# Performance work log

Hardware: AMD Instinct MI355X
Metric: run time of the kernel (lower is better)

The kernel has to match this reference:

```python
import jax, jax.numpy as jnp
import numpy as np

ANCHORS = jnp.array([[0.57273, 0.677385], [1.87446, 2.06253], [3.33843, 5.47434],
                     [7.88282, 3.52778], [9.77052, 9.16828]], dtype=jnp.float32)
IOU_THR = 0.6
SCALE_NOOBJ = 1.0
SCALE_OBJ = 5.0
DS = 32.0          # downsample_rate
EPS = 1e-7


def _iou_wh(w1, h1, w2, h2):
    # GetCenterAlignIouBetween: boxes aligned at centers -> IoU depends on w,h only
    inter = jnp.minimum(w1, w2) * jnp.minimum(h1, h2)
    return inter / (w1 * h1 + w2 * h2 - inter + EPS)


def setup_inputs() -> dict:
    B, W, H, A, C, M = 128, 19, 19, 5, 81, 24
    N = W * H
    key = jax.random.key(0)
    ks = jax.random.split(key, 8)
    ii, jj = jnp.meshgrid(jnp.arange(W), jnp.arange(H), indexing='ij')
    fm_cord = jnp.stack([jj, ii], -1).reshape(N, 2).astype(jnp.float32)  # (x=j, y=i)
    conf = jax.random.uniform(ks[0], (B, W, H, A, 1)) * 0.98 + 0.01      # valid BCE probs
    pred_xy = fm_cord.reshape(1, W, H, 1, 2) + jax.random.uniform(ks[1], (B, W, H, A, 2))
    pred_wh = jax.random.uniform(ks[2], (B, W, H, A, 2)) * 8.0 + 0.2     # fm units, >0
    cls_score = jax.random.normal(ks[3], (B, W, H, A, C))
    # distinct grid cells per image so sequential scatter == vectorized scatter
    cells = jax.vmap(lambda k: jax.random.choice(k, N, (M,), replace=False))(
        jax.random.split(ks[4], B))
    ci = cells // H
    cj = cells % H
    frac = jax.random.uniform(ks[5], (B, M, 2))
    x = (cj.astype(jnp.float32) + frac[..., 0]) * DS   # pixel coords
    y = (ci.astype(jnp.float32) + frac[..., 1]) * DS
    wh = jax.random.uniform(ks[6], (B, M, 2), minval=12.0, maxval=280.0)
    true_object = jnp.stack([x, y, wh[..., 0], wh[..., 1]], -1)          # [B,M,4] pixels
    labels = jax.random.randint(ks[7], (B, M), 0, C - 1)
    true_label = jax.nn.one_hot(labels, C, dtype=jnp.float32)            # [B,M,C]
    return dict(epoch=0, conf=conf, pred_xy=pred_xy, pred_wh=pred_wh,
                cls_score=cls_score, true_label=true_label,
                true_object=true_object, fm_cord=fm_cord)


def _yolo_loss(conf, pred_xy, pred_wh, cls_score, true_label, true_object, fm_cord):
    B, W, H, A, C = cls_score.shape
    N = W * H
    NA = N * A
    S = float(W)  # config.output_size

    # ---- target assignment (vectorized version of the python loops) ----
    obj = true_object / DS                               # fm units, [B,M,4]
    gx, gy, gw, gh = obj[..., 0], obj[..., 1], obj[..., 2], obj[..., 3]
    i = gy.astype(jnp.int32)                             # row index  (int() truncation)
    j = gx.astype(jnp.int32)                             # col index
    cell = i * H + j                                     # flat cell, [B,M]

    a_iou = _iou_wh(ANCHORS[None, None, :, 0], ANCHORS[None, None, :, 1],
                    gw[..., None], gh[..., None])        # [B,M,A]
    best = jnp.argmax(a_iou, axis=-1)                    # [B,M]
    is_best = best[..., None] == jnp.arange(A)[None, None, :]
    over = a_iou > IOU_THR

    bb = jnp.arange(B)[:, None]
    pwh = pred_wh.reshape(B, N, A, 2)[bb, cell]          # [B,M,A,2] gather at gt cells
    pwh_b = jnp.take_along_axis(pwh, best[..., None, None], axis=2)[:, :, 0]  # [B,M,2]
    iou_pg = _iou_wh(pwh_b[..., 0], pwh_b[..., 1], gw, gh)                    # [B,M]

    mask_val = jnp.where(is_best, 1.0, jnp.where(over, -1.0, 0.0))            # [B,M,A]
    sw = 2.0 - (gw / S) * (gh / S)                                            # [B,M]
    sw_val = jnp.where(is_best, sw[..., None], jnp.where(over, -1.0, 0.0))
    pgi_val = jnp.where(~is_best & over, 0.0, iou_pg[..., None])              # [B,M,A]
    bg = jax.nn.one_hot(C - 1, C, dtype=cls_score.dtype)
    ts_val = jnp.where((is_best | over)[..., None], true_label[:, :, None, :], bg)
    bbox_val = jnp.where(is_best[..., None], obj[:, :, None, :], 0.0)         # [B,M,A,4]

    obj_mask = jnp.zeros((B, N, A)).at[bb, cell].set(mask_val)
    scale_w = jnp.zeros((B, N, A)).at[bb, cell].set(sw_val)
    pgi = jnp.zeros((B, N, A)).at[bb, cell].set(pgi_val)
    true_score = jnp.zeros((B, N, A, C)).at[..., -1].set(1.0).at[bb, cell].set(ts_val)
    true_bbox = jnp.zeros((B, N, A, 4)).at[bb, cell].set(bbox_val)

    # ---- masked losses over flattened [B, W*H*A, ...] ----
    conf_f = conf.reshape(B, NA)
    om = obj_mask.reshape(B, NA)
    swf = scale_w.reshape(B, NA)
    pgif = pgi.reshape(B, NA)
    pxy = pred_xy.reshape(B, NA, 2)
    pwh_f = pred_wh.reshape(B, NA, 2)
    tb = true_bbox.reshape(B, NA, 4)
    ts = true_score.reshape(B, NA, C)
    cs = cls_score.reshape(B, NA, C)
    cord = jnp.repeat(fm_cord[:, None, :], A, axis=1).reshape(NA, 2)

    cp = jnp.clip(conf_f, EPS, 1.0 - EPS)
    noobj_loss = SCALE_NOOBJ * jnp.sum((om == 0) * (-jnp.log(1.0 - cp))) / B
    obj_loss = SCALE_OBJ * jnp.sum(
        (om == 1) * (-(pgif * jnp.log(cp) + (1.0 - pgif) * jnp.log(1.0 - cp)))) / B

    gt = (swf > 0).astype(conf_f.dtype)                  # [B,NA]
    w3 = (SCALE_OBJ * gt * swf)[..., None]
    xy_loss = jnp.sum(w3 * ((pxy - cord[None]) - (tb[..., :2] - cord[None])) ** 2) / B
    wh_loss = jnp.sum(w3 * (pwh_f - tb[..., 2:]) ** 2) / B

    # CE with soft targets, per position: [B,NA]
    ce = -jnp.sum(ts * jax.nn.log_softmax(cs, axis=-1), axis=-1)
    # original broadcasts mask [B,1,NA] * ce [B,NA] -> [B,B,NA] then .sum();
    # equivalent factored form: sum_n (sum_b1 mask) * (sum_b2 ce)
    score_loss = SCALE_OBJ * jnp.sum(gt.sum(0) * ce.sum(0)) / B

    total = noobj_loss + obj_loss + xy_loss + wh_loss + score_loss
    return total, noobj_loss, obj_loss, score_loss, xy_loss, wh_loss


def reference(epoch, conf, pred_xy, pred_wh, cls_score, true_label, true_object, fm_cord):
    return _yolo_loss(conf, pred_xy, pred_wh, cls_score,
                      true_label, true_object, fm_cord)
```

## Files before the change

kernel.cpp:

```cpp
#include <hip/hip_runtime.h>

#define Bsz 128
#define Cd 81
#define Md 24
#define Nd 361
#define NAd 1805
#define RPW 16
#define NT 113
#define NBLK_CLS (NT*16)
#define NOBJ (Bsz*Md)
#define NBLK_LAB (NOBJ/RPW)
#define EPSF 1e-7f
#define IOU_THRF 0.6f

#define OFF_CORR  0
#define OFF_GT    1824
#define OFF_ACC   3648
#define MEMSET_FLOATS 3652
#define OFF_PART  4096
#define OFF_NOOBJ 33024
#define OFF_LAB   35072

#define EXP4(v) { v.x=__expf(v.x); v.y=__expf(v.y); v.z=__expf(v.z); v.w=__expf(v.w); }

__global__ __launch_bounds__(64) void yolo_sweep(
        const float* __restrict__ conf,
        const float* __restrict__ cls_score,
        const float* __restrict__ true_label,
        float* __restrict__ ws) {
    __shared__ float ex[1300];
    const int lane = threadIdx.x;
    const int r = lane >> 2, h = lane & 3;
    const int bid = blockIdx.x;
    float4* l4 = (float4*)ex;

    if (bid < NBLK_CLS) {
        const int t = bid >> 4, g = bid & 15;
        const int na0 = (t == NT - 1) ? (NAd - RPW) : t * RPW;
        const int vmin = t * RPW;
        const bool validr = (na0 + r) >= vmin;
        const bool validc = (lane < RPW) && ((na0 + lane) >= vmin);

        float accCE = 0.0f, nb = 0.0f;

        size_t s = ((size_t)(g * 8) * NAd + na0) * Cd;
        size_t a0 = s & ~(size_t)3;
        int mcur = (int)(s & 3);
        const float4* gp = (const float4*)cls_score + (a0 >> 2);
        float4 u0 = gp[0 * 64 + lane];
        float4 u1 = gp[1 * 64 + lane];
        float4 u2 = gp[2 * 64 + lane];
        float4 u3 = gp[3 * 64 + lane];
        float4 u4 = gp[4 * 64 + lane];
        float4 u5 = gp[261 + lane];
        float cf = validc ? conf[(size_t)(g * 8) * NAd + na0 + lane] : 0.5f;

        for (int it = 0; it < 8; ++it) {
            EXP4(u0); EXP4(u1); EXP4(u2); EXP4(u3); EXP4(u4); EXP4(u5);
            l4[0 * 64 + lane] = u0;
            l4[1 * 64 + lane] = u1;
            l4[2 * 64 + lane] = u2;
            l4[3 * 64 + lane] = u3;
            l4[4 * 64 + lane] = u4;
            l4[261 + lane] = u5;
            __builtin_amdgcn_wave_barrier();

            float4 n0 = {}, n1 = {}, n2 = {}, n3 = {}, n4 = {}, n5 = {};
            float cfn = 0.0f; int mnext = 0;
            if (it < 7) {
                int b = g * 8 + it + 1;
                s = ((size_t)b * NAd + na0) * Cd;
                a0 = s & ~(size_t)3;
                mnext = (int)(s & 3);
                gp = (const float4*)cls_score + (a0 >> 2);
                n0 = gp[0 * 64 + lane];
                n1 = gp[1 * 64 + lane];
                n2 = gp[2 * 64 + lane];
                n3 = gp[3 * 64 + lane];
                n4 = gp[4 * 64 + lane];
                n5 = gp[261 + lane];
                cfn = validc ? conf[(size_t)b * NAd + na0 + lane] : 0.5f;
            }

            const float* p = ex + mcur + r * Cd;
            float sacc = 0.0f;
            #pragma unroll
            for (int j = 0; j < 21; j++) {
                int c0 = h * 21 + j;
                int cc = c0 < 81 ? c0 : 80;
                float w = (c0 < 81) ? 1.0f : 0.0f;
                sacc += p[cc] * w;
            }
            sacc += __shfl_xor(sacc, 1, 64);
            sacc += __shfl_xor(sacc, 2, 64);
            if (h == 0 && validr)
                accCE += __logf(sacc) - __logf(p[80]);
            if (validc) {
                float cp = fminf(fmaxf(cf, EPSF), 1.0f - EPSF);
                nb += -__logf(1.0f - cp);
            }

            u0 = n0; u1 = n1; u2 = n2; u3 = n3; u4 = n4; u5 = n5;
            cf = cfn; mcur = mnext;
        }

        if (h == 0 && validr)
            ws[OFF_PART + (size_t)(na0 + r) * 16 + g] = accCE;

        #pragma unroll
        for (int off = 32; off > 0; off >>= 1) nb += __shfl_xor(nb, off, 64);
        if (lane == 0) ws[OFF_NOOBJ + bid] = nb;
    } else {
        const int lb = bid - NBLK_CLS;
        const float4* gp = (const float4*)(true_label + (size_t)lb * (RPW * Cd));
        float4 u0 = gp[0 * 64 + lane];
        float4 u1 = gp[1 * 64 + lane];
        float4 u2 = gp[2 * 64 + lane];
        float4 u3 = gp[3 * 64 + lane];
        float4 u4 = gp[4 * 64 + lane];
        float4 u5 = gp[260 + lane];
        l4[0 * 64 + lane] = u0;
        l4[1 * 64 + lane] = u1;
        l4[2 * 64 + lane] = u2;
        l4[3 * 64 + lane] = u3;
        l4[4 * 64 + lane] = u4;
        l4[260 + lane] = u5;
        __builtin_amdgcn_wave_barrier();
        const float* p = ex + r * Cd;
        float sacc = 0.0f;
        #pragma unroll
        for (int j = 0; j < 21; j++) {
            int c0 = h * 21 + j;
            int cc = c0 < 81 ? c0 : 80;
            float w = (c0 < 81) ? (float)c0 : 0.0f;
            sacc += p[cc] * w;
        }
        sacc += __shfl_xor(sacc, 1, 64);
        sacc += __shfl_xor(sacc, 2, 64);
        if (h == 0) ws[OFF_LAB + lb * RPW + r] = sacc;
    }
}

__global__ __launch_bounds__(64) void yolo_assign(
        const float* __restrict__ conf,
        const float* __restrict__ pred_xy,
        const float* __restrict__ pred_wh,
        const float* __restrict__ cls_score,
        const float* __restrict__ true_object,
        float* __restrict__ ws) {
    const float AW[5] = {0.57273f, 1.87446f, 3.33843f, 7.88282f, 9.77052f};
    const float AH[5] = {0.677385f, 2.06253f, 5.47434f, 3.52778f, 9.16828f};
    const int idx = blockIdx.x * 64 + threadIdx.x;
    float* corr = ws + OFF_CORR;
    float* gt   = ws + OFF_GT;

    int lab = (int)(ws[OFF_LAB + idx] + 0.5f);
    int b = idx / Md;
    const float4 to = ((const float4*)true_object)[idx];
    const float inv_ds = 1.0f / 32.0f;
    float gx = to.x * inv_ds, gy = to.y * inv_ds;
    float gw = to.z * inv_ds, gh = to.w * inv_ds;
    int ci = (int)gy, cj = (int)gx;
    int cell = ci * 19 + cj;
    float garea = gw * gh;

    float best_iou = -1.0f; int best = 0; bool over[5];
    #pragma unroll
    for (int a = 0; a < 5; a++) {
        float inter = fminf(AW[a], gw) * fminf(AH[a], gh);
        float iou = inter / (AW[a] * AH[a] + garea - inter + EPSF);
        over[a] = iou > IOU_THRF;
        if (iou > best_iou) { best_iou = iou; best = a; }
    }

    int base_bn = (b * Nd + cell) * 5;
    float pwb = pred_wh[(size_t)(base_bn + best) * 2 + 0];
    float phb = pred_wh[(size_t)(base_bn + best) * 2 + 1];
    float inter = fminf(pwb, gw) * fminf(phb, gh);
    float iou_pg = inter / (pwb * phb + garea - inter + EPSF);
    float sw = 2.0f - (gw * (1.0f / 19.0f)) * (gh * (1.0f / 19.0f));

    float a0 = 0.f, a1 = 0.f, a2 = 0.f, a3 = 0.f;
    #pragma unroll
    for (int a = 0; a < 5; a++) {
        bool isb = (a == best);
        if (!(isb || over[a])) continue;
        int pos = base_bn + a;
        int na  = cell * 5 + a;
        float cp = fminf(fmaxf(conf[pos], EPSF), 1.0f - EPSF);
        a0 += __logf(1.0f - cp);
        const float* cs = cls_score + (size_t)pos * Cd;
        atomicAdd(&corr[na], cs[Cd - 1] - cs[lab]);
        if (isb) {
            atomicAdd(&gt[na], 1.0f);
            a1 += -(iou_pg * __logf(cp) + (1.0f - iou_pg) * __logf(1.0f - cp));
            float px = pred_xy[(size_t)pos * 2 + 0], py = pred_xy[(size_t)pos * 2 + 1];
            a2 += sw * ((px - gx) * (px - gx) + (py - gy) * (py - gy));
            float pwa = pred_wh[(size_t)pos * 2 + 0], pha = pred_wh[(size_t)pos * 2 + 1];
            a3 += sw * ((pwa - gw) * (pwa - gw) + (pha - gh) * (pha - gh));
        }
    }

    #pragma unroll
    for (int off = 32; off > 0; off >>= 1) {
        a0 += __shfl_xor(a0, off, 64);
        a1 += __shfl_xor(a1, off, 64);
        a2 += __shfl_xor(a2, off, 64);
        a3 += __shfl_xor(a3, off, 64);
    }
    if (threadIdx.x == 0) {
        atomicAdd(&ws[OFF_ACC + 0], a0);
        atomicAdd(&ws[OFF_ACC + 1], a1);
        atomicAdd(&ws[OFF_ACC + 2], a2);
        atomicAdd(&ws[OFF_ACC + 3], a3);
    }
}

__global__ __launch_bounds__(1024) void yolo_reduce(
        const float* __restrict__ ws, float* __restrict__ out) {
    __shared__ float red[2][16];
    const int tid = threadIdx.x;
    float nsum = 0.0f;
    for (int i = tid; i < NBLK_CLS; i += 1024) nsum += ws[OFF_NOOBJ + i];
    float ssum = 0.0f;
    const float4* part4 = (const float4*)(ws + OFF_PART);
    for (int na = tid; na < NAd; na += 1024) {
        float4 p0 = part4[na * 4 + 0];
        float4 p1 = part4[na * 4 + 1];
        float4 p2 = part4[na * 4 + 2];
        float4 p3 = part4[na * 4 + 3];
        float ce = p0.x + p0.y + p0.z + p0.w + p1.x + p1.y + p1.z + p1.w
                 + p2.x + p2.y + p2.z + p2.w + p3.x + p3.y + p3.z + p3.w
                 + ws[OFF_CORR + na];
        ssum += ws[OFF_GT + na] * ce;
    }

    float v[2] = {nsum, ssum};
    #pragma unroll
    for (int k = 0; k < 2; k++) {
        float x = v[k];
        #pragma unroll
        for (int off = 32; off > 0; off >>= 1) x += __shfl_xor(x, off, 64);
        if ((tid & 63) == 0) red[k][tid >> 6] = x;
    }
    __syncthreads();
    if (tid == 0) {
        float t0 = 0.f, t1 = 0.f;
        #pragma unroll
        for (int w = 0; w < 16; w++) { t0 += red[0][w]; t1 += red[1][w]; }
        const float invB = 1.0f / (float)Bsz;
        float noobj = 1.0f * (t0 + ws[OFF_ACC + 0]) * invB;
        float obj   = 5.0f * ws[OFF_ACC + 1] * invB;
        float xy    = 5.0f * ws[OFF_ACC + 2] * invB;
        float wh    = 5.0f * ws[OFF_ACC + 3] * invB;
        float score = 5.0f * t1 * invB;
        out[0] = noobj + obj + xy + wh + score;
        out[1] = noobj;
        out[2] = obj;
        out[3] = score;
        out[4] = xy;
        out[5] = wh;
    }
}

extern "C" void kernel_launch(void* const* d_in, const int* in_sizes, int n_in,
                              void* d_out, int out_size, void* d_ws, size_t ws_size,
                              hipStream_t stream) {
    const float* conf    = (const float*)d_in[1];
    const float* pred_xy = (const float*)d_in[2];
    const float* pred_wh = (const float*)d_in[3];
    const float* cls     = (const float*)d_in[4];
    const float* tlabel  = (const float*)d_in[5];
    const float* tobject = (const float*)d_in[6];
    float* ws  = (float*)d_ws;
    float* out = (float*)d_out;

    hipMemsetAsync(ws, 0, MEMSET_FLOATS * sizeof(float), stream);

    yolo_sweep<<<NBLK_CLS + NBLK_LAB, 64, 0, stream>>>(conf, cls, tlabel, ws);

    yolo_assign<<<NOBJ / 64, 64, 0, stream>>>(conf, pred_xy, pred_wh, cls, tobject, ws);

    yolo_reduce<<<1, 1024, 0, stream>>>(ws, out);
}
```

Measured before the change: 131.7 us.

## Fuse target assignment into sweep kernel and halve per-block batch group

Merges the assign kernel into the class-score sweep kernel as leading blocks, computing each object's label index directly from its one-hot row instead of through a separate label-decoding pass and workspace buffer. This removes one kernel launch and the dependency between label decode and assignment. The sweep now covers 4 images per block instead of 8, doubling the block count to 32 groups per tile, with the partial-sum layout and final reduction widened to match. Each assign thread now reads a full 81-float label row serially with uncoalesced strided access. Smaller groups give more parallelism but less prefetch pipelining per block.

```diff
diff --git a/kernel.cpp b/kernel.cpp
--- a/kernel.cpp
+++ b/kernel.cpp
@@ -7,9 +7,11 @@
 #define NAd 1805
 #define RPW 16
 #define NT 113
-#define NBLK_CLS (NT*16)
+#define GPB 4
+#define NGRP 32
+#define NBLK_CLS (NT*NGRP)
 #define NOBJ (Bsz*Md)
-#define NBLK_LAB (NOBJ/RPW)
+#define NBLK_ASSIGN (NOBJ/64)
 #define EPSF 1e-7f
 #define IOU_THRF 0.6f
 
@@ -18,24 +20,27 @@
 #define OFF_ACC   3648
 #define MEMSET_FLOATS 3652
 #define OFF_PART  4096
-#define OFF_NOOBJ 33024
-#define OFF_LAB   35072
+#define OFF_NOOBJ 61952
 
 #define EXP4(v) { v.x=__expf(v.x); v.y=__expf(v.y); v.z=__expf(v.z); v.w=__expf(v.w); }
 
-__global__ __launch_bounds__(64) void yolo_sweep(
+__global__ __launch_bounds__(64) void yolo_main(
         const float* __restrict__ conf,
+        const float* __restrict__ pred_xy,
+        const float* __restrict__ pred_wh,
         const float* __restrict__ cls_score,
         const float* __restrict__ true_label,
+        const float* __restrict__ true_object,
         float* __restrict__ ws) {
     __shared__ float ex[1300];
     const int lane = threadIdx.x;
-    const int r = lane >> 2, h = lane & 3;
     const int bid = blockIdx.x;
-    float4* l4 = (float4*)ex;
-
-    if (bid < NBLK_CLS) {
-        const int t = bid >> 4, g = bid & 15;
+
+    if (bid >= NBLK_ASSIGN) {
+        const int cb = bid - NBLK_ASSIGN;
+        const int t = cb >> 5, g = cb & 31;
+        const int r = lane >> 2, h = lane & 3;
+        float4* l4 = (float4*)ex;
         const int na0 = (t == NT - 1) ? (NAd - RPW) : t * RPW;
         const int vmin = t * RPW;
         const bool validr = (na0 + r) >= vmin;
@@ -43,7 +48,7 @@
 
         float accCE = 0.0f, nb = 0.0f;
 
-        size_t s = ((size_t)(g * 8) * NAd + na0) * Cd;
+        size_t s = ((size_t)(g * GPB) * NAd + na0) * Cd;
         size_t a0 = s & ~(size_t)3;
         int mcur = (int)(s & 3);
         const float4* gp = (const float4*)cls_score + (a0 >> 2);
@@ -53,9 +58,9 @@
         float4 u3 = gp[3 * 64 + lane];
         float4 u4 = gp[4 * 64 + lane];
         float4 u5 = gp[261 + lane];
-        float cf = validc ? conf[(size_t)(g * 8) * NAd + na0 + lane] : 0.5f;
-
-        for (int it = 0; it < 8; ++it) {
+        float cf = validc ? conf[(size_t)(g * GPB) * NAd + na0 + lane] : 0.5f;
+
+        for (int it = 0; it < GPB; ++it) {
             EXP4(u0); EXP4(u1); EXP4(u2); EXP4(u3); EXP4(u4); EXP4(u5);
             l4[0 * 64 + lane] = u0;
             l4[1 * 64 + lane] = u1;
@@ -67,8 +72,8 @@
 
             float4 n0 = {}, n1 = {}, n2 = {}, n3 = {}, n4 = {}, n5 = {};
             float cfn = 0.0f; int mnext = 0;
-            if (it < 7) {
-                int b = g * 8 + it + 1;
+            if (it < GPB - 1) {
+                int b = g * GPB + it + 1;
                 s = ((size_t)b * NAd + na0) * Cd;
                 a0 = s & ~(size_t)3;
                 mnext = (int)(s & 3);
@@ -105,114 +110,83 @@
         }
 
         if (h == 0 && validr)
-            ws[OFF_PART + (size_t)(na0 + r) * 16 + g] = accCE;
+            ws[OFF_PART + (size_t)(na0 + r) * NGRP + g] = accCE;
 
         #pragma unroll
         for (int off = 32; off > 0; off >>= 1) nb += __shfl_xor(nb, off, 64);
-        if (lane == 0) ws[OFF_NOOBJ + bid] = nb;
+        if (lane == 0) ws[OFF_NOOBJ + cb] = nb;
     } else {
-        const int lb = bid - NBLK_CLS;
-        const float4* gp = (const float4*)(true_label + (size_t)lb * (RPW * Cd));
-        float4 u0 = gp[0 * 64 + lane];
-        float4 u1 = gp[1 * 64 + lane];
-        float4 u2 = gp[2 * 64 + lane];
-        float4 u3 = gp[3 * 64 + lane];
-        float4 u4 = gp[4 * 64 + lane];
-        float4 u5 = gp[260 + lane];
-        l4[0 * 64 + lane] = u0;
-        l4[1 * 64 + lane] = u1;
-        l4[2 * 64 + lane] = u2;
-        l4[3 * 64 + lane] = u3;
-        l4[4 * 64 + lane] = u4;
-        l4[260 + lane] = u5;
-        __builtin_amdgcn_wave_barrier();
-        const float* p = ex + r * Cd;
-        float sacc = 0.0f;
-        #pragma unroll
-        for (int j = 0; j < 21; j++) {
-            int c0 = h * 21 + j;
-            int cc = c0 < 81 ? c0 : 80;
-            float w = (c0 < 81) ? (float)c0 : 0.0f;
-            sacc += p[cc] * w;
-        }
-        sacc += __shfl_xor(sacc, 1, 64);
-        sacc += __shfl_xor(sacc, 2, 64);
-        if (h == 0) ws[OFF_LAB + lb * RPW + r] = sacc;
-    }
-}
-
-__global__ __launch_bounds__(64) void yolo_assign(
-        const float* __restrict__ conf,
-        const float* __restrict__ pred_xy,
-        const float* __restrict__ pred_wh,
-        const float* __restrict__ cls_score,
-        const float* __restrict__ true_object,
-        float* __restrict__ ws) {
-    const float AW[5] = {0.57273f, 1.87446f, 3.33843f, 7.88282f, 9.77052f};
-    const float AH[5] = {0.677385f, 2.06253f, 5.47434f, 3.52778f, 9.16828f};
-    const int idx = blockIdx.x * 64 + threadIdx.x;
-    float* corr = ws + OFF_CORR;
-    float* gt   = ws + OFF_GT;
-
-    int lab = (int)(ws[OFF_LAB + idx] + 0.5f);
-    int b = idx / Md;
-    const float4 to = ((const float4*)true_object)[idx];
-    const float inv_ds = 1.0f / 32.0f;
-    float gx = to.x * inv_ds, gy = to.y * inv_ds;
-    float gw = to.z * inv_ds, gh = to.w * inv_ds;
-    int ci = (int)gy, cj = (int)gx;
-    int cell = ci * 19 + cj;
-    float garea = gw * gh;
-
-    float best_iou = -1.0f; int best = 0; bool over[5];
-    #pragma unroll
-    for (int a = 0; a < 5; a++) {
-        float inter = fminf(AW[a], gw) * fminf(AH[a], gh);
-        float iou = inter / (AW[a] * AH[a] + garea - inter + EPSF);
-        over[a] = iou > IOU_THRF;
-        if (iou > best_iou) { best_iou = iou; best = a; }
-    }
-
-    int base_bn = (b * Nd + cell) * 5;
-    float pwb = pred_wh[(size_t)(base_bn + best) * 2 + 0];
-    float phb = pred_wh[(size_t)(base_bn + best) * 2 + 1];
-    float inter = fminf(pwb, gw) * fminf(phb, gh);
-    float iou_pg = inter / (pwb * phb + garea - inter + EPSF);
-    float sw = 2.0f - (gw * (1.0f / 19.0f)) * (gh * (1.0f / 19.0f));
-
-    float a0 = 0.f, a1 = 0.f, a2 = 0.f, a3 = 0.f;
-    #pragma unroll
-    for (int a = 0; a < 5; a++) {
-        bool isb = (a == best);
-        if (!(isb || over[a])) continue;
-        int pos = base_bn + a;
-        int na  = cell * 5 + a;
-        float cp = fminf(fmaxf(conf[pos], EPSF), 1.0f - EPSF);
-        a0 += __logf(1.0f - cp);
-        const float* cs = cls_score + (size_t)pos * Cd;
-        atomicAdd(&corr[na], cs[Cd - 1] - cs[lab]);
-        if (isb) {
-            atomicAdd(&gt[na], 1.0f);
-            a1 += -(iou_pg * __logf(cp) + (1.0f - iou_pg) * __logf(1.0f - cp));
-            float px = pred_xy[(size_t)pos * 2 + 0], py = pred_xy[(size_t)pos * 2 + 1];
-            a2 += sw * ((px - gx) * (px - gx) + (py - gy) * (py - gy));
-            float pwa = pred_wh[(size_t)pos * 2 + 0], pha = pred_wh[(size_t)pos * 2 + 1];
-            a3 += sw * ((pwa - gw) * (pwa - gw) + (pha - gh) * (pha - gh));
-        }
-    }
-
-    #pragma unroll
-    for (int off = 32; off > 0; off >>= 1) {
-        a0 += __shfl_xor(a0, off, 64);
-        a1 += __shfl_xor(a1, off, 64);
-        a2 += __shfl_xor(a2, off, 64);
-        a3 += __shfl_xor(a3, off, 64);
-    }
-    if (threadIdx.x == 0) {
-        atomicAdd(&ws[OFF_ACC + 0], a0);
-        atomicAdd(&ws[OFF_ACC + 1], a1);
-        atomicAdd(&ws[OFF_ACC + 2], a2);
-        atomicAdd(&ws[OFF_ACC + 3], a3);
+        const float AW[5] = {0.57273f, 1.87446f, 3.33843f, 7.88282f, 9.77052f};
+        const float AH[5] = {0.677385f, 2.06253f, 5.47434f, 3.52778f, 9.16828f};
+        const int idx = bid * 64 + lane;
+        float* corr = ws + OFF_CORR;
+        float* gt   = ws + OFF_GT;
+
+        const float* lrow = true_label + (size_t)idx * Cd;
+        float labf = 0.0f;
+        #pragma unroll
+        for (int c = 1; c < Cd; c++) labf += lrow[c] * (float)c;
+        int lab = (int)(labf + 0.5f);
+
+        int b = idx / Md;
+        const float4 to = ((const float4*)true_object)[idx];
+        const float inv_ds = 1.0f / 32.0f;
+        float gx = to.x * inv_ds, gy = to.y * inv_ds;
+        float gw = to.z * inv_ds, gh = to.w * inv_ds;
+        int ci = (int)gy, cj = (int)gx;
+        int cell = ci * 19 + cj;
+        float garea = gw * gh;
+
+        float best_iou = -1.0f; int best = 0; bool over[5];
+        #pragma unroll
+        for (int a = 0; a < 5; a++) {
+            float inter = fminf(AW[a], gw) * fminf(AH[a], gh);
+            float iou = inter / (AW[a] * AH[a] + garea - inter + EPSF);
+            over[a] = iou > IOU_THRF;
+            if (iou > best_iou) { best_iou = iou; best = a; }
+        }
+
+        int base_bn = (b * Nd + cell) * 5;
+        float pwb = pred_wh[(size_t)(base_bn + best) * 2 + 0];
+        float phb = pred_wh[(size_t)(base_bn + best) * 2 + 1];
+        float inter = fminf(pwb, gw) * fminf(phb, gh);
+        float iou_pg = inter / (pwb * phb + garea - inter + EPSF);
+        float sw = 2.0f - (gw * (1.0f / 19.0f)) * (gh * (1.0f / 19.0f));
+
+        float a0 = 0.f, a1 = 0.f, a2 = 0.f, a3 = 0.f;
+        #pragma unroll
+        for (int a = 0; a < 5; a++) {
+            bool isb = (a == best);
+            if (!(isb || over[a])) continue;
+            int pos = base_bn + a;
+            int na  = cell * 5 + a;
+            float cp = fminf(fmaxf(conf[pos], EPSF), 1.0f - EPSF);
+            a0 += __logf(1.0f - cp);
+            const float* cs = cls_score + (size_t)pos * Cd;
+            atomicAdd(&corr[na], cs[Cd - 1] - cs[lab]);
+            if (isb) {
+                atomicAdd(&gt[na], 1.0f);
+                a1 += -(iou_pg * __logf(cp) + (1.0f - iou_pg) * __logf(1.0f - cp));
+                float px = pred_xy[(size_t)pos * 2 + 0], py = pred_xy[(size_t)pos * 2 + 1];
+                a2 += sw * ((px - gx) * (px - gx) + (py - gy) * (py - gy));
+                float pwa = pred_wh[(size_t)pos * 2 + 0], pha = pred_wh[(size_t)pos * 2 + 1];
+                a3 += sw * ((pwa - gw) * (pwa - gw) + (pha - gh) * (pha - gh));
+            }
+        }
+
+        #pragma unroll
+        for (int off = 32; off > 0; off >>= 1) {
+            a0 += __shfl_xor(a0, off, 64);
+            a1 += __shfl_xor(a1, off, 64);
+            a2 += __shfl_xor(a2, off, 64);
+            a3 += __shfl_xor(a3, off, 64);
+        }
+        if (lane == 0) {
+            atomicAdd(&ws[OFF_ACC + 0], a0);
+            atomicAdd(&ws[OFF_ACC + 1], a1);
+            atomicAdd(&ws[OFF_ACC + 2], a2);
+            atomicAdd(&ws[OFF_ACC + 3], a3);
+        }
     }
 }
 
@@ -225,13 +199,14 @@
     float ssum = 0.0f;
     const float4* part4 = (const float4*)(ws + OFF_PART);
     for (int na = tid; na < NAd; na += 1024) {
-        float4 p0 = part4[na * 4 + 0];
-        float4 p1 = part4[na * 4 + 1];
-        float4 p2 = part4[na * 4 + 2];
-        float4 p3 = part4[na * 4 + 3];
-        float ce = p0.x + p0.y + p0.z + p0.w + p1.x + p1.y + p1.z + p1.w
-                 + p2.x + p2.y + p2.z + p2.w + p3.x + p3.y + p3.z + p3.w
-                 + ws[OFF_CORR + na];
+        const float4* p4 = part4 + (size_t)na * 8;
+        float ce = 0.0f;
+        #pragma unroll
+        for (int k = 0; k < 8; k++) {
+            float4 q = p4[k];
+            ce += q.x + q.y + q.z + q.w;
+        }
+        ce += ws[OFF_CORR + na];
         ssum += ws[OFF_GT + na] * ce;
     }
 
@@ -277,9 +252,8 @@
 
     hipMemsetAsync(ws, 0, MEMSET_FLOATS * sizeof(float), stream);
 
-    yolo_sweep<<<NBLK_CLS + NBLK_LAB, 64, 0, stream>>>(conf, cls, tlabel, ws);
-
-    yolo_assign<<<NOBJ / 64, 64, 0, stream>>>(conf, pred_xy, pred_wh, cls, tobject, ws);
+    yolo_main<<<NBLK_ASSIGN + NBLK_CLS, 64, 0, stream>>>(
+        conf, pred_xy, pred_wh, cls, tlabel, tobject, ws);
 
     yolo_reduce<<<1, 1024, 0, stream>>>(ws, out);
 }
```

Measured after the change: 131.8 us (median of 2 runs). Within noise of the previous version (+0.0%).
